# Performance work log

Measured on AMD Instinct MI355X. Metric: run time of the kernel, lower is better.

Reference implementation:

```python
import jax, jax.numpy as jnp
import numpy as np

B, S, N, E = 8, 32, 2000, 64000
GH, H = 32, 64  # gat_h, lstm hidden
NEG_SLOPE = 0.2


def setup_inputs() -> dict:
    key = jax.random.key(0)
    ks = jax.random.split(key, 12)
    f32 = jnp.float32
    x = jax.random.normal(ks[0], (B, S, N), f32)
    edge_index = jax.random.randint(ks[1], (2, E), 0, N)
    # GATConv(1, GH, heads=1, concat=False): lin weight [GH,1] -> vector, att_src/att_dst [GH], bias [GH]
    w_lin = jax.random.normal(ks[2], (GH,), f32)
    att_src = jax.random.normal(ks[3], (GH,), f32) * 0.1
    att_dst = jax.random.normal(ks[4], (GH,), f32) * 0.1
    gat_bias = jax.random.normal(ks[5], (GH,), f32) * 0.01
    D = GH * N  # LSTM input size
    W_ih = jax.random.normal(ks[6], (4 * H, D), f32) * (1.0 / np.sqrt(D))
    W_hh = jax.random.normal(ks[7], (4 * H, H), f32) * (1.0 / np.sqrt(H))
    b_ih = jax.random.normal(ks[8], (4 * H,), f32) * 0.01
    b_hh = jax.random.normal(ks[9], (4 * H,), f32) * 0.01
    W_head = jax.random.normal(ks[10], (N, H), f32) * (1.0 / np.sqrt(H))
    b_head = jax.random.normal(ks[11], (N,), f32) * 0.01
    return {"x": x, "edge_index": edge_index, "w_lin": w_lin, "att_src": att_src,
            "att_dst": att_dst, "gat_bias": gat_bias, "W_ih": W_ih, "W_hh": W_hh,
            "b_ih": b_ih, "b_hh": b_hh, "W_head": W_head, "b_head": b_head}


def reference(x, edge_index, w_lin, att_src, att_dst, gat_bias,
              W_ih, W_hh, b_ih, b_hh, W_head, b_head):
    x = x.astype(jnp.float32)
    # --- GAT (in_channels=1, heads=1), batched over (B,S) ---
    # PyG default: add self-loops
    loops = jnp.arange(N)
    ei = jnp.concatenate([edge_index, jnp.stack([loops, loops])], axis=1)
    src, dst = ei[0], ei[1]  # [Et], Et = E + N
    # lifted feature h_n = x_n * w_lin (rank-1), so attention logits are scalar per node
    a_src = x * jnp.dot(w_lin, att_src)  # [B,S,N]
    a_dst = x * jnp.dot(w_lin, att_dst)  # [B,S,N]
    e = jax.nn.leaky_relu(a_src[..., src] + a_dst[..., dst], NEG_SLOPE)  # [B,S,Et]
    e = jnp.moveaxis(e, -1, 0)  # [Et,B,S] (segment axis leading)
    seg_max = jax.ops.segment_max(e, dst, num_segments=N)  # [N,B,S]
    e = jnp.exp(e - seg_max[dst])
    denom = jax.ops.segment_sum(e, dst, num_segments=N)  # [N,B,S]
    alpha = e / denom[dst]  # edge softmax over incoming edges
    x_src = jnp.moveaxis(x[..., src], -1, 0)  # [Et,B,S]
    agg = jax.ops.segment_sum(alpha * x_src, dst, num_segments=N)  # [N,B,S]
    agg = jnp.moveaxis(agg, 0, -1)  # [B,S,N]
    # outer product with w_lin restores [.,GH]; add bias, then relu (from forward)
    h = jax.nn.relu(agg[..., None] * w_lin + gat_bias)  # [B,S,N,GH]
    lstm_in = h.reshape(B, S, N * GH)

    # --- LSTM (1 layer, batch_first), keep final hidden state ---
    def step(carry, xt):
        hp, cp = carry
        gates = xt @ W_ih.T + b_ih + hp @ W_hh.T + b_hh  # [B,4H]
        i, f, g, o = jnp.split(gates, 4, axis=-1)
        c = jax.nn.sigmoid(f) * cp + jax.nn.sigmoid(i) * jnp.tanh(g)
        hn = jax.nn.sigmoid(o) * jnp.tanh(c)
        return (hn, c), None

    h0 = jnp.zeros((B, H), jnp.float32)
    c0 = jnp.zeros((B, H), jnp.float32)
    (hT, _), _ = jax.lax.scan(step, (h0, c0), jnp.swapaxes(lstm_in, 0, 1))
    return hT @ W_head.T + b_head  # [B,N]
```

## Files before the change

kernel.cpp:

```cpp
#include <hip/hip_runtime.h>
#include <hip/hip_bf16.h>
#include <cstddef>
#include <cstdint>

#define B_  8
#define S_  32
#define BT_ 256
#define N_  2000
#define E_  64000
#define GH_ 32
#define H_  64
#define G4_ 256
#define D_  64000
#define NEG_SLOPE_ 0.2f
#define KC_  64

typedef __attribute__((ext_vector_type(8))) _Float16 half8;
typedef __attribute__((ext_vector_type(4))) float floatx4;

__device__ __forceinline__ float fsigmoid(float x) { return 1.0f / (1.0f + __expf(-x)); }
__device__ __forceinline__ float ftanh_(float x)   { return 1.0f - 2.0f / (__expf(2.0f * x) + 1.0f); }

__global__ __launch_bounds__(256) void k_prep(
    const float* __restrict__ x, float* __restrict__ xT, int* __restrict__ deg)
{
  const int gt = blockIdx.x * 256 + threadIdx.x;
  if (gt < N_) deg[gt] = 0;

  __shared__ float tile[32][33];
  const int TXT = (N_ + 31) / 32;
  const int t = blockIdx.x;
  if (t >= TXT * (BT_ / 32)) return;
  const int tx = threadIdx.x & 31;
  const int ty = threadIdx.x >> 5;
  const int n0  = (t % TXT) * 32;
  const int bt0 = (t / TXT) * 32;
#pragma unroll
  for (int r = 0; r < 4; ++r) {
    const int bt = bt0 + ty + r * 8;
    const int nn = n0 + tx;
    if (nn < N_) tile[ty + r * 8][tx] = x[(size_t)bt * N_ + nn];
  }
  __syncthreads();
#pragma unroll
  for (int r = 0; r < 4; ++r) {
    const int n = n0 + ty + r * 8;
    if (n < N_) xT[(size_t)n * BT_ + bt0 + tx] = tile[tx][ty + r * 8];
  }
}

__global__ __launch_bounds__(256) void k_hist(
    const int* __restrict__ ei, int* __restrict__ deg)
{
  const int i = blockIdx.x * 256 + threadIdx.x;
  if (i < E_) atomicAdd(&deg[ei[E_ + i]], 1);
}

__global__ __launch_bounds__(256) void k_scan(
    const int* __restrict__ deg, int* __restrict__ rowptr, int* __restrict__ cursor)
{
  __shared__ int tsum[256];
  const int tid = threadIdx.x;
  int v[8];
  int s = 0;
  const int base = tid * 8;
#pragma unroll
  for (int j = 0; j < 8; ++j) {
    const int idx = base + j;
    const int d = (idx < N_) ? deg[idx] : 0;
    v[j] = s;
    s += d;
  }
  tsum[tid] = s;
  __syncthreads();
  for (int off = 1; off < 256; off <<= 1) {
    int t = 0;
    if (tid >= off) t = tsum[tid - off];
    __syncthreads();
    tsum[tid] += t;
    __syncthreads();
  }
  const int ebase = tsum[tid] - s;
#pragma unroll
  for (int j = 0; j < 8; ++j) {
    const int idx = base + j;
    if (idx < N_) {
      const int r = ebase + v[j];
      rowptr[idx] = r;
      cursor[idx] = r;
    }
  }
  if (tid == 0) rowptr[N_] = E_;
}

__global__ __launch_bounds__(256) void k_scatter(
    const int* __restrict__ ei, int* __restrict__ cursor, int* __restrict__ csr_src)
{
  const int i = blockIdx.x * 256 + threadIdx.x;
  if (i >= E_) return;
  const int s = ei[i];
  const int d = ei[E_ + i];
  const int pos = atomicAdd(&cursor[d], 1);
  csr_src[pos] = s;
}

__global__ __launch_bounds__(256) void k_gather(
    const float* __restrict__ xT, const int* __restrict__ rowptr,
    const int* __restrict__ csr_src,
    const float* __restrict__ w_lin, const float* __restrict__ att_src,
    const float* __restrict__ att_dst, float* __restrict__ agg)
{
  const int n   = blockIdx.x;
  const int tid = threadIdx.x;
  float c_s = 0.f, c_d = 0.f;
  for (int g = 0; g < GH_; ++g) {
    const float w = w_lin[g];
    c_s += w * att_src[g];
    c_d += w * att_dst[g];
  }
  const int r0 = rowptr[n];
  const int d  = rowptr[n + 1] - r0;
  const float xn = xT[(size_t)n * BT_ + tid];
  const float cdxn = c_d * xn;
  float e = (c_s + c_d) * xn;
  e = e > 0.f ? e : NEG_SLOPE_ * e;
  const float w0 = __expf(e);
  float num = w0 * xn, den = w0;
  int pp = 0;
  for (; pp + 4 <= d; pp += 4) {
    const int s0 = csr_src[r0 + pp + 0];
    const int s1 = csr_src[r0 + pp + 1];
    const int s2 = csr_src[r0 + pp + 2];
    const int s3 = csr_src[r0 + pp + 3];
    const float x0 = xT[(size_t)s0 * BT_ + tid];
    const float x1 = xT[(size_t)s1 * BT_ + tid];
    const float x2 = xT[(size_t)s2 * BT_ + tid];
    const float x3 = xT[(size_t)s3 * BT_ + tid];
    float e0 = fmaf(c_s, x0, cdxn); e0 = e0 > 0.f ? e0 : NEG_SLOPE_ * e0;
    float e1 = fmaf(c_s, x1, cdxn); e1 = e1 > 0.f ? e1 : NEG_SLOPE_ * e1;
    float e2 = fmaf(c_s, x2, cdxn); e2 = e2 > 0.f ? e2 : NEG_SLOPE_ * e2;
    float e3 = fmaf(c_s, x3, cdxn); e3 = e3 > 0.f ? e3 : NEG_SLOPE_ * e3;
    const float w0_ = __expf(e0), w1_ = __expf(e1), w2_ = __expf(e2), w3_ = __expf(e3);
    num += w0_ * x0 + w1_ * x1 + w2_ * x2 + w3_ * x3;
    den += (w0_ + w1_) + (w2_ + w3_);
  }
  for (; pp < d; ++pp) {
    const int s = csr_src[r0 + pp];
    const float xs = xT[(size_t)s * BT_ + tid];
    float ee = fmaf(c_s, xs, cdxn);
    ee = ee > 0.f ? ee : NEG_SLOPE_ * ee;
    const float ww = __expf(ee);
    num += ww * xs;
    den += ww;
  }
  agg[(size_t)n * BT_ + tid] = num / den;
}

__global__ __launch_bounds__(256) void k_mfma(
    const float* __restrict__ W_ih, const float* __restrict__ agg,
    const float* __restrict__ w_lin, const float* __restrict__ gat_bias,
    float* __restrict__ partial)
{
  const int nb = blockIdx.x;
  const int kc = blockIdx.y;
  const int n0 = (N_ * kc) / KC_;
  const int n1 = (N_ * (kc + 1)) / KC_;
  const int tid  = threadIdx.x;
  const int wv   = tid >> 6;
  const int lane = tid & 63;
  const int i16  = lane & 15;
  const int q    = lane >> 4;
  const int j0   = nb * 32;

  float wlq[8], gbq[8];
#pragma unroll
  for (int j = 0; j < 8; ++j) {
    wlq[j] = w_lin[q * 8 + j];
    gbq[j] = gat_bias[q * 8 + j];
  }

  floatx4 acc[4][2];
#pragma unroll
  for (int mt = 0; mt < 4; ++mt)
#pragma unroll
    for (int nt = 0; nt < 2; ++nt)
#pragma unroll
      for (int r = 0; r < 4; ++r) acc[mt][nt][r] = 0.f;

  const float* Bp0 = W_ih + (size_t)(j0 + i16) * D_ + (size_t)n0 * GH_ + q * 8;
  const float* Bp1 = Bp0 + (size_t)16 * D_;

  float4 c0a = *(const float4*)(Bp0);
  float4 c0b = *(const float4*)(Bp0 + 4);
  float4 c1a = *(const float4*)(Bp1);
  float4 c1b = *(const float4*)(Bp1 + 4);

#pragma unroll 1
  for (int nn = n0; nn < n1; ++nn) {
    const int nx = (nn + 1 < n1) ? (nn + 1 - n0) : (nn - n0);
    const int off = nx * GH_;
    float4 p0a = *(const float4*)(Bp0 + off);
    float4 p0b = *(const float4*)(Bp0 + off + 4);
    float4 p1a = *(const float4*)(Bp1 + off);
    float4 p1b = *(const float4*)(Bp1 + off + 4);

    half8 bf0, bf1;
    bf0[0] = (_Float16)c0a.x; bf0[1] = (_Float16)c0a.y;
    bf0[2] = (_Float16)c0a.z; bf0[3] = (_Float16)c0a.w;
    bf0[4] = (_Float16)c0b.x; bf0[5] = (_Float16)c0b.y;
    bf0[6] = (_Float16)c0b.z; bf0[7] = (_Float16)c0b.w;
    bf1[0] = (_Float16)c1a.x; bf1[1] = (_Float16)c1a.y;
    bf1[2] = (_Float16)c1a.z; bf1[3] = (_Float16)c1a.w;
    bf1[4] = (_Float16)c1b.x; bf1[5] = (_Float16)c1b.y;
    bf1[6] = (_Float16)c1b.z; bf1[7] = (_Float16)c1b.w;

    const float* Ar = agg + (size_t)nn * BT_ + wv * 64 + i16;
#pragma unroll
    for (int mt = 0; mt < 4; ++mt) {
      const float a = Ar[mt * 16];
      half8 af;
#pragma unroll
      for (int j = 0; j < 8; ++j) {
        float v = fmaf(a, wlq[j], gbq[j]);
        v = fmaxf(v, 0.f);
        af[j] = (_Float16)v;
      }
      acc[mt][0] = __builtin_amdgcn_mfma_f32_16x16x32_f16(af, bf0, acc[mt][0], 0, 0, 0);
      acc[mt][1] = __builtin_amdgcn_mfma_f32_16x16x32_f16(af, bf1, acc[mt][1], 0, 0, 0);
    }
    c0a = p0a; c0b = p0b; c1a = p1a; c1b = p1b;
  }

#pragma unroll
  for (int mt = 0; mt < 4; ++mt) {
    const int bt = wv * 64 + mt * 16 + q * 4;
#pragma unroll
    for (int nt = 0; nt < 2; ++nt) {
      const int j = j0 + nt * 16 + i16;
#pragma unroll
      for (int r = 0; r < 4; ++r)
        partial[(size_t)kc * 65536 + (size_t)(bt + r) * G4_ + j] = acc[mt][nt][r];
    }
  }
}

__global__ __launch_bounds__(256) void k_reduce(
    const float* __restrict__ partial, float* __restrict__ pre_gates)
{
  const int o = blockIdx.x * 256 + threadIdx.x;
  float s0 = 0.f, s1 = 0.f, s2 = 0.f, s3 = 0.f;
#pragma unroll
  for (int kc = 0; kc < KC_; kc += 4) {
    s0 += partial[(size_t)(kc + 0) * 65536 + o];
    s1 += partial[(size_t)(kc + 1) * 65536 + o];
    s2 += partial[(size_t)(kc + 2) * 65536 + o];
    s3 += partial[(size_t)(kc + 3) * 65536 + o];
  }
  pre_gates[o] = (s0 + s1) + (s2 + s3);
}

__global__ __launch_bounds__(256) void k_lstm_head(
    const float* __restrict__ pre_gates, const float* __restrict__ W_hh,
    const float* __restrict__ b_ih, const float* __restrict__ b_hh,
    const float* __restrict__ W_head, const float* __restrict__ b_head,
    float* __restrict__ out)
{
  const int b   = blockIdx.x;
  const int tid = threadIdx.x;
  __shared__ float h_s[H_];
  __shared__ float g_s[G4_];

  float wr[H_];
#pragma unroll
  for (int k = 0; k < H_; ++k) wr[k] = W_hh[(size_t)tid * H_ + k];
  float pg[S_];
#pragma unroll
  for (int t = 0; t < S_; ++t) pg[t] = pre_gates[(size_t)(b * S_ + t) * G4_ + tid];

  const float bias = b_ih[tid] + b_hh[tid];
  if (tid < H_) h_s[tid] = 0.f;
  float c = 0.f;
  __syncthreads();

  for (int t = 0; t < S_; ++t) {
    float g0 = pg[t] + bias, g1 = 0.f, g2 = 0.f, g3 = 0.f;
#pragma unroll
    for (int k = 0; k < H_; k += 4) {
      g0 = fmaf(wr[k + 0], h_s[k + 0], g0);
      g1 = fmaf(wr[k + 1], h_s[k + 1], g1);
      g2 = fmaf(wr[k + 2], h_s[k + 2], g2);
      g3 = fmaf(wr[k + 3], h_s[k + 3], g3);
    }
    g_s[tid] = (g0 + g1) + (g2 + g3);
    __syncthreads();
    if (tid < H_) {
      const float ig = fsigmoid(g_s[tid]);
      const float fg = fsigmoid(g_s[H_ + tid]);
      const float gg = ftanh_(g_s[2 * H_ + tid]);
      const float og = fsigmoid(g_s[3 * H_ + tid]);
      c = fg * c + ig * gg;
      h_s[tid] = og * ftanh_(c);
    }
    __syncthreads();
  }

  for (int n = tid; n < N_; n += 256) {
    const float4* w4 = (const float4*)(W_head + (size_t)n * H_);
    float acc = b_head[n];
#pragma unroll
    for (int qq = 0; qq < H_ / 4; ++qq) {
      const float4 w = w4[qq];
      acc += w.x * h_s[qq * 4 + 0] + w.y * h_s[qq * 4 + 1] +
             w.z * h_s[qq * 4 + 2] + w.w * h_s[qq * 4 + 3];
    }
    out[(size_t)b * N_ + n] = acc;
  }
}

extern "C" void kernel_launch(void* const* d_in, const int* in_sizes, int n_in,
                              void* d_out, int out_size, void* d_ws, size_t ws_size,
                              hipStream_t stream) {
  const float* x        = (const float*)d_in[0];
  const int*   ei       = (const int*)  d_in[1];
  const float* w_lin    = (const float*)d_in[2];
  const float* att_src  = (const float*)d_in[3];
  const float* att_dst  = (const float*)d_in[4];
  const float* gat_bias = (const float*)d_in[5];
  const float* W_ih     = (const float*)d_in[6];
  const float* W_hh     = (const float*)d_in[7];
  const float* b_ih     = (const float*)d_in[8];
  const float* b_hh     = (const float*)d_in[9];
  const float* W_head   = (const float*)d_in[10];
  const float* b_head   = (const float*)d_in[11];
  float* out = (float*)d_out;

  char* ws = (char*)d_ws;
  float* xT        = (float*)(ws + 0);
  float* agg       = (float*)(ws + 2048000);
  float* pre_gates = (float*)(ws + 4096000);
  int*   deg       = (int*)  (ws + 4358144);
  int*   rowptr    = (int*)  (ws + 4366336);
  int*   cursor    = (int*)  (ws + 4374528);
  int*   csr_src   = (int*)  (ws + 4382720);
  float* partial   = (float*)(ws + 4638720);

  k_prep<<<dim3(504), dim3(256), 0, stream>>>(x, xT, deg);
  k_hist<<<dim3((E_ + 255) / 256), dim3(256), 0, stream>>>(ei, deg);
  k_scan<<<dim3(1), dim3(256), 0, stream>>>(deg, rowptr, cursor);
  k_scatter<<<dim3((E_ + 255) / 256), dim3(256), 0, stream>>>(ei, cursor, csr_src);
  k_gather<<<dim3(N_), dim3(256), 0, stream>>>(
      xT, rowptr, csr_src, w_lin, att_src, att_dst, agg);
  k_mfma<<<dim3(8, KC_), dim3(256), 0, stream>>>(
      W_ih, agg, w_lin, gat_bias, partial);
  k_reduce<<<dim3(256), dim3(256), 0, stream>>>(partial, pre_gates);
  k_lstm_head<<<dim3(B_), dim3(256), 0, stream>>>(
      pre_gates, W_hh, b_ih, b_hh, W_head, b_head, out);
}
```

Before: 261.5 us.

## Stage aggregated node features in LDS and double-buffer two W_ih nodes per iteration

Result: slower. 283.9 us (+8.6%).

```diff
diff --git a/kernel.cpp b/kernel.cpp
--- a/kernel.cpp
+++ b/kernel.cpp
@@ -13,7 +13,8 @@
 #define G4_ 256
 #define D_  64000
 #define NEG_SLOPE_ 0.2f
-#define KC_  64
+#define KC_  63
+#define NPC_ 32
 
 typedef __attribute__((ext_vector_type(8))) _Float16 half8;
 typedef __attribute__((ext_vector_type(4))) float floatx4;
@@ -161,10 +162,11 @@
     const float* __restrict__ w_lin, const float* __restrict__ gat_bias,
     float* __restrict__ partial)
 {
+  __shared__ float As[NPC_ * BT_];
   const int nb = blockIdx.x;
   const int kc = blockIdx.y;
-  const int n0 = (N_ * kc) / KC_;
-  const int n1 = (N_ * (kc + 1)) / KC_;
+  const int n0 = kc * NPC_;
+  const int nNodes = (N_ - n0 < NPC_) ? (N_ - n0) : NPC_;
   const int tid  = threadIdx.x;
   const int wv   = tid >> 6;
   const int lane = tid & 63;
@@ -172,6 +174,13 @@
   const int q    = lane >> 4;
   const int j0   = nb * 32;
 
+  {
+    const float4* src = (const float4*)(agg + (size_t)n0 * BT_);
+    float4* dst = (float4*)As;
+    const int nv = nNodes * (BT_ / 4);
+    for (int i = tid; i < nv; i += 256) dst[i] = src[i];
+  }
+
   float wlq[8], gbq[8];
 #pragma unroll
   for (int j = 0; j < 8; ++j) {
@@ -187,48 +196,57 @@
 #pragma unroll
       for (int r = 0; r < 4; ++r) acc[mt][nt][r] = 0.f;
 
+  __syncthreads();
+
   const float* Bp0 = W_ih + (size_t)(j0 + i16) * D_ + (size_t)n0 * GH_ + q * 8;
   const float* Bp1 = Bp0 + (size_t)16 * D_;
 
-  float4 c0a = *(const float4*)(Bp0);
-  float4 c0b = *(const float4*)(Bp0 + 4);
-  float4 c1a = *(const float4*)(Bp1);
-  float4 c1b = *(const float4*)(Bp1 + 4);
-
-#pragma unroll 1
-  for (int nn = n0; nn < n1; ++nn) {
-    const int nx = (nn + 1 < n1) ? (nn + 1 - n0) : (nn - n0);
-    const int off = nx * GH_;
-    float4 p0a = *(const float4*)(Bp0 + off);
-    float4 p0b = *(const float4*)(Bp0 + off + 4);
-    float4 p1a = *(const float4*)(Bp1 + off);
-    float4 p1b = *(const float4*)(Bp1 + off + 4);
-
+  auto ldB = [&](float4* v, int nn) {
+    const size_t off = (size_t)nn * GH_;
+    v[0] = *(const float4*)(Bp0 + off);
+    v[1] = *(const float4*)(Bp0 + off + 4);
+    v[2] = *(const float4*)(Bp1 + off);
+    v[3] = *(const float4*)(Bp1 + off + 4);
+  };
+  auto compute = [&](const float4* v, int nnl) {
     half8 bf0, bf1;
-    bf0[0] = (_Float16)c0a.x; bf0[1] = (_Float16)c0a.y;
-    bf0[2] = (_Float16)c0a.z; bf0[3] = (_Float16)c0a.w;
-    bf0[4] = (_Float16)c0b.x; bf0[5] = (_Float16)c0b.y;
-    bf0[6] = (_Float16)c0b.z; bf0[7] = (_Float16)c0b.w;
-    bf1[0] = (_Float16)c1a.x; bf1[1] = (_Float16)c1a.y;
-    bf1[2] = (_Float16)c1a.z; bf1[3] = (_Float16)c1a.w;
-    bf1[4] = (_Float16)c1b.x; bf1[5] = (_Float16)c1b.y;
-    bf1[6] = (_Float16)c1b.z; bf1[7] = (_Float16)c1b.w;
-
-    const float* Ar = agg + (size_t)nn * BT_ + wv * 64 + i16;
+    bf0[0] = (_Float16)v[0].x; bf0[1] = (_Float16)v[0].y;
+    bf0[2] = (_Float16)v[0].z; bf0[3] = (_Float16)v[0].w;
+    bf0[4] = (_Float16)v[1].x; bf0[5] = (_Float16)v[1].y;
+    bf0[6] = (_Float16)v[1].z; bf0[7] = (_Float16)v[1].w;
+    bf1[0] = (_Float16)v[2].x; bf1[1] = (_Float16)v[2].y;
+    bf1[2] = (_Float16)v[2].z; bf1[3] = (_Float16)v[2].w;
+    bf1[4] = (_Float16)v[3].x; bf1[5] = (_Float16)v[3].y;
+    bf1[6] = (_Float16)v[3].z; bf1[7] = (_Float16)v[3].w;
 #pragma unroll
     for (int mt = 0; mt < 4; ++mt) {
-      const float a = Ar[mt * 16];
+      const float a = As[nnl * BT_ + wv * 64 + mt * 16 + i16];
       half8 af;
 #pragma unroll
       for (int j = 0; j < 8; ++j) {
-        float v = fmaf(a, wlq[j], gbq[j]);
-        v = fmaxf(v, 0.f);
-        af[j] = (_Float16)v;
+        float val = fmaf(a, wlq[j], gbq[j]);
+        val = fmaxf(val, 0.f);
+        af[j] = (_Float16)val;
       }
       acc[mt][0] = __builtin_amdgcn_mfma_f32_16x16x32_f16(af, bf0, acc[mt][0], 0, 0, 0);
       acc[mt][1] = __builtin_amdgcn_mfma_f32_16x16x32_f16(af, bf1, acc[mt][1], 0, 0, 0);
     }
-    c0a = p0a; c0b = p0b; c1a = p1a; c1b = p1b;
+  };
+
+  float4 cur0[4], cur1[4], nxt0[4], nxt1[4];
+  ldB(cur0, 0);
+  ldB(cur1, 1);
+
+#pragma unroll 1
+  for (int nn = 0; nn < nNodes; nn += 2) {
+    const int nx0 = (nn + 2 < nNodes) ? nn + 2 : nn;
+    const int nx1 = (nn + 3 < nNodes) ? nn + 3 : nn + 1;
+    ldB(nxt0, nx0);
+    ldB(nxt1, nx1);
+    compute(cur0, nn);
+    compute(cur1, nn + 1);
+#pragma unroll
+    for (int i = 0; i < 4; ++i) { cur0[i] = nxt0[i]; cur1[i] = nxt1[i]; }
   }
 
 #pragma unroll
@@ -248,15 +266,14 @@
     const float* __restrict__ partial, float* __restrict__ pre_gates)
 {
   const int o = blockIdx.x * 256 + threadIdx.x;
-  float s0 = 0.f, s1 = 0.f, s2 = 0.f, s3 = 0.f;
-#pragma unroll
-  for (int kc = 0; kc < KC_; kc += 4) {
+  float s0 = 0.f, s1 = 0.f, s2 = 0.f;
+#pragma unroll
+  for (int kc = 0; kc < KC_; kc += 3) {
     s0 += partial[(size_t)(kc + 0) * 65536 + o];
     s1 += partial[(size_t)(kc + 1) * 65536 + o];
     s2 += partial[(size_t)(kc + 2) * 65536 + o];
-    s3 += partial[(size_t)(kc + 3) * 65536 + o];
-  }
-  pre_gates[o] = (s0 + s1) + (s2 + s3);
+  }
+  pre_gates[o] = s0 + s1 + s2;
 }
 
 __global__ __launch_bounds__(256) void k_lstm_head(
```
